# Kernel tuning notes

Hardware: AMD Instinct MI355X
Metric: run time of the kernel (lower is better)

Reference implementation:

```python
import jax, jax.numpy as jnp
import numpy as np


def setup_inputs() -> dict:
    key = jax.random.key(0)
    kq, kk, kv = jax.random.split(key, 3)
    B, S, D = 4, 4096, 64
    q = jax.random.normal(kq, (B, S, D), dtype=jnp.float32)
    k = jax.random.normal(kk, (B, S, D), dtype=jnp.float32)
    v = jax.random.normal(kv, (B, S, D), dtype=jnp.float32)
    return {"q": q, "k": k, "v": v}


def reference(q, k, v):
    # q,k,v: [B,S,D]. Faithful to the torch module:
    #   attn = softmax(q @ k^T / sqrt(D))  -- softmax over full row (NOT pre-masked)
    #   attn = attn.masked_fill(tril==0, 0.0)  -- post-softmax causal zeroing
    #   out  = attn @ v
    S = q.shape[1]
    d = jnp.sqrt(jnp.asarray(q.shape[-1], dtype=q.dtype))
    scores = jnp.einsum("bqd,bkd->bqk", q, k) / d  # [B,S,S]
    attn = jax.nn.softmax(scores, axis=-1)
    # causal tril mask sliced from the registered buffer mask[:S,:S]
    causal = jnp.tril(jnp.ones((S, S), dtype=bool))  # [S,S]
    attn = jnp.where(causal[None, :, :], attn, jnp.asarray(0.0, dtype=attn.dtype))
    out = jnp.einsum("bqk,bkd->bqd", attn, v)  # [B,S,D]
    return out
```

## Files before the change

kernel.cpp:

```cpp
#include <hip/hip_runtime.h>
#include <math.h>


typedef _Float16 f16;
typedef __attribute__((ext_vector_type(8))) _Float16 f16x8;
typedef __attribute__((ext_vector_type(16))) float f32x16;

constexpr int S = 4096, D = 64, TK = 32;
constexpr int B_ = 4;
constexpr int NKT = S / TK;
constexpr int QB = 32;
constexpr int WPB = 8;
constexpr int TPW = NKT / WPB;
constexpr int LDV = 40;
constexpr float QSC = 0.125f * 1.44269504088896340736f;

__global__ __launch_bounds__(256) void prep(
    const float* __restrict__ K, const float* __restrict__ V,
    f16* __restrict__ Kfrag, f16* __restrict__ Vfrag) {
  const int bx = blockIdx.x, tid = threadIdx.x;
  if (bx < B_ * NKT) {
    const float* src = K + (size_t)bx * TK * D;
    const int key = tid >> 3, j = tid & 7;
    float4 f0 = *reinterpret_cast<const float4*>(src + key * D + j * 8);
    float4 f1 = *reinterpret_cast<const float4*>(src + key * D + j * 8 + 4);
    f16x8 h;
    h[0] = (f16)f0.x; h[1] = (f16)f0.y; h[2] = (f16)f0.z; h[3] = (f16)f0.w;
    h[4] = (f16)f1.x; h[5] = (f16)f1.y; h[6] = (f16)f1.z; h[7] = (f16)f1.w;
    const int kc = j >> 1, h2 = j & 1;
    const int lane = key + 32 * h2;
    *reinterpret_cast<f16x8*>(Kfrag + ((size_t)bx * 4 + kc) * 512 + lane * 8) = h;
  } else {
    __shared__ float t32[TK][D + 4];
    const int vb = bx - B_ * NKT;
    const float* src = V + (size_t)vb * TK * D;
    #pragma unroll
    for (int r = 0; r < 2; ++r) {
      int f4 = tid + r * 256;
      int row = f4 >> 4, c4 = (f4 & 15) * 4;
      *reinterpret_cast<float4*>(&t32[row][c4]) =
          *reinterpret_cast<const float4*>(src + row * D + c4);
    }
    __syncthreads();
    const int dn = tid >> 7, kc2 = (tid >> 6) & 1, lane = tid & 63;
    const int l31 = lane & 31, h2 = lane >> 5;
    const int dim = dn * 32 + l31;
    const int k0 = kc2 * 16 + 8 * h2;
    f16x8 h;
    #pragma unroll
    for (int jj = 0; jj < 8; ++jj) h[jj] = (f16)t32[k0 + jj][dim];
    *reinterpret_cast<f16x8*>(
        Vfrag + ((size_t)vb * 4 + dn * 2 + kc2) * 512 + lane * 8) = h;
  }
}

__global__ __launch_bounds__(512, 4)
void attn(const float* __restrict__ Q, const f16* __restrict__ Kfrag,
          const f16* __restrict__ Vfrag, float* __restrict__ O) {
  __shared__ union {
    f16 ps[WPB][QB][LDV];
    struct { float nb[4][QB][68]; float db[WPB][QB]; } r;
  } sm;

  const int i = blockIdx.x;
  const int b = (i & 7) >> 1;
  const int t = ((i >> 3) << 1) | (i & 1);
  const int qb = (t & 1) ? (127 - (t >> 1)) : (t >> 1);
  const int q0 = qb * QB;

  const int tid = threadIdx.x;
  const int w = tid >> 6, lane = tid & 63;
  const int l31 = lane & 31, h2 = lane >> 5;

  const size_t bSD = (size_t)b * S * D;

  f16x8 qh[4], qlo[4];
  {
    const float* qr = Q + bSD + (size_t)(q0 + l31) * D;
    #pragma unroll
    for (int kc = 0; kc < 4; ++kc) {
      float4 f0 = *reinterpret_cast<const float4*>(qr + kc * 16 + 8 * h2);
      float4 f1 = *reinterpret_cast<const float4*>(qr + kc * 16 + 8 * h2 + 4);
      float f[8] = {f0.x, f0.y, f0.z, f0.w, f1.x, f1.y, f1.z, f1.w};
      #pragma unroll
      for (int j = 0; j < 8; ++j) {
        float v = f[j] * QSC;
        f16 hi = (f16)v;
        qh[kc][j] = hi;
        qlo[kc][j] = (f16)(v - (float)hi);
      }
    }
  }

  const f16* kf = Kfrag + (size_t)b * NKT * 2048 + lane * 8;
  const f16* vf = Vfrag + (size_t)b * NKT * 2048 + lane * 8;

  f32x16 on0, on1;
  float ls[16];
  #pragma unroll
  for (int r = 0; r < 16; ++r) { on0[r] = 0.f; on1[r] = 0.f; ls[r] = 0.f; }

  for (int j = 0; j < TPW; ++j) {
    const int kt = (j << 3) | w;
    const int kbase = kt * TK;
    const bool pv = (kbase <= q0);
    const bool diag = (kbase == q0);

    f16x8 v00, v01, v10, v11;
    if (pv) {
      const f16* vp = vf + (size_t)kt * 2048;
      v00 = *reinterpret_cast<const f16x8*>(vp);
      v01 = *reinterpret_cast<const f16x8*>(vp + 512);
      v10 = *reinterpret_cast<const f16x8*>(vp + 1024);
      v11 = *reinterpret_cast<const f16x8*>(vp + 1536);
    }

    const f16* kp = kf + (size_t)kt * 2048;
    f16x8 bk0 = *reinterpret_cast<const f16x8*>(kp);
    f16x8 bk1 = *reinterpret_cast<const f16x8*>(kp + 512);
    f16x8 bk2 = *reinterpret_cast<const f16x8*>(kp + 1024);
    f16x8 bk3 = *reinterpret_cast<const f16x8*>(kp + 1536);

    f32x16 acc;
    #pragma unroll
    for (int r = 0; r < 16; ++r) acc[r] = 0.f;
    acc = __builtin_amdgcn_mfma_f32_32x32x16_f16(qlo[0], bk0, acc, 0, 0, 0);
    acc = __builtin_amdgcn_mfma_f32_32x32x16_f16(qh[0],  bk0, acc, 0, 0, 0);
    acc = __builtin_amdgcn_mfma_f32_32x32x16_f16(qlo[1], bk1, acc, 0, 0, 0);
    acc = __builtin_amdgcn_mfma_f32_32x32x16_f16(qh[1],  bk1, acc, 0, 0, 0);
    acc = __builtin_amdgcn_mfma_f32_32x32x16_f16(qlo[2], bk2, acc, 0, 0, 0);
    acc = __builtin_amdgcn_mfma_f32_32x32x16_f16(qh[2],  bk2, acc, 0, 0, 0);
    acc = __builtin_amdgcn_mfma_f32_32x32x16_f16(qlo[3], bk3, acc, 0, 0, 0);
    acc = __builtin_amdgcn_mfma_f32_32x32x16_f16(qh[3],  bk3, acc, 0, 0, 0);

    #pragma unroll
    for (int r = 0; r < 16; ++r) {
      float pp = __builtin_amdgcn_exp2f(acc[r]);
      f16 ph = (f16)pp;
      ls[r] += (float)ph;
      if (pv) {
        const int row = (r & 3) + 8 * (r >> 2) + 4 * h2;
        sm.ps[w][row][l31] = (!diag || l31 <= row) ? ph : (f16)0.f;
      }
    }

    if (pv) {
      asm volatile("s_waitcnt lgkmcnt(0)" ::: "memory");
      f16x8 ap0 = *reinterpret_cast<const f16x8*>(&sm.ps[w][l31][8 * h2]);
      f16x8 ap1 = *reinterpret_cast<const f16x8*>(&sm.ps[w][l31][16 + 8 * h2]);
      on0 = __builtin_amdgcn_mfma_f32_32x32x16_f16(ap0, v00, on0, 0, 0, 0);
      on0 = __builtin_amdgcn_mfma_f32_32x32x16_f16(ap1, v01, on0, 0, 0, 0);
      on1 = __builtin_amdgcn_mfma_f32_32x32x16_f16(ap0, v10, on1, 0, 0, 0);
      on1 = __builtin_amdgcn_mfma_f32_32x32x16_f16(ap1, v11, on1, 0, 0, 0);
    }
  }

  #pragma unroll
  for (int r = 0; r < 16; ++r) {
    float v = ls[r];
    #pragma unroll
    for (int x = 1; x <= 16; x <<= 1) v += __shfl_xor(v, x);
    ls[r] = v;
  }
  __syncthreads();
  if (l31 == 0) {
    #pragma unroll
    for (int r = 0; r < 16; ++r)
      sm.r.db[w][(r & 3) + 8 * (r >> 2) + 4 * h2] = ls[r];
  }
  if (w < 4) {
    #pragma unroll
    for (int r = 0; r < 16; ++r) {
      const int row = (r & 3) + 8 * (r >> 2) + 4 * h2;
      sm.r.nb[w][row][l31]      = on0[r];
      sm.r.nb[w][row][32 + l31] = on1[r];
    }
  }
  __syncthreads();
  if (w >= 4) {
    #pragma unroll
    for (int r = 0; r < 16; ++r) {
      const int row = (r & 3) + 8 * (r >> 2) + 4 * h2;
      sm.r.nb[w - 4][row][l31]      += on0[r];
      sm.r.nb[w - 4][row][32 + l31] += on1[r];
    }
  }
  __syncthreads();

  const int row = tid >> 4, c4 = (tid & 15) * 4;
  float dsum = 0.f;
  #pragma unroll
  for (int ww = 0; ww < WPB; ++ww) dsum += sm.r.db[ww][row];
  const float inv = 1.f / dsum;
  float4 a0 = *reinterpret_cast<const float4*>(&sm.r.nb[0][row][c4]);
  float4 a1 = *reinterpret_cast<const float4*>(&sm.r.nb[1][row][c4]);
  float4 a2 = *reinterpret_cast<const float4*>(&sm.r.nb[2][row][c4]);
  float4 a3 = *reinterpret_cast<const float4*>(&sm.r.nb[3][row][c4]);
  float4 o;
  o.x = (a0.x + a1.x + a2.x + a3.x) * inv;
  o.y = (a0.y + a1.y + a2.y + a3.y) * inv;
  o.z = (a0.z + a1.z + a2.z + a3.z) * inv;
  o.w = (a0.w + a1.w + a2.w + a3.w) * inv;
  *reinterpret_cast<float4*>(O + bSD + (size_t)(q0 + row) * D + c4) = o;
}

extern "C" void kernel_launch(void* const* d_in, const int* in_sizes, int n_in,
                              void* d_out, int out_size, void* d_ws, size_t ws_size,
                              hipStream_t stream) {
  const float* q = (const float*)d_in[0];
  const float* k = (const float*)d_in[1];
  const float* v = (const float*)d_in[2];
  float* o = (float*)d_out;

  f16* Kfrag = (f16*)d_ws;
  f16* Vfrag = Kfrag + (size_t)B_ * S * D;

  prep<<<dim3(2 * B_ * NKT), dim3(256), 0, stream>>>(k, v, Kfrag, Vfrag);
  attn<<<dim3(512), dim3(512), 0, stream>>>(q, Kfrag, Vfrag, o);
}
```

Baseline: 111.3 us.

## Merge paired causal query tiles into one 1024-thread block

Each block now handles two 32-row query tiles, a low one and its mirrored high one (g and 127-g), with 16 waves. Waves alternate between the two tiles, and each half splits the key tiles across eight waves. The grid shrinks from 512 to 256 blocks, about one per CU, so the causal workload is balanced inside each block rather than across blocks. In exchange, the final reduction runs in two serialized passes with extra barriers, and the larger launch bound may tighten register limits.

```diff
diff --git a/kernel.cpp b/kernel.cpp
--- a/kernel.cpp
+++ b/kernel.cpp
@@ -9,9 +9,8 @@
 constexpr int S = 4096, D = 64, TK = 32;
 constexpr int B_ = 4;
 constexpr int NKT = S / TK;
-constexpr int QB = 32;
-constexpr int WPB = 8;
-constexpr int TPW = NKT / WPB;
+constexpr int WPB = 16;
+constexpr int TPW = 16;
 constexpr int LDV = 40;
 constexpr float QSC = 0.125f * 1.44269504088896340736f;
 
@@ -54,23 +53,25 @@
   }
 }
 
-__global__ __launch_bounds__(512, 4)
+__global__ __launch_bounds__(1024, 4)
 void attn(const float* __restrict__ Q, const f16* __restrict__ Kfrag,
           const f16* __restrict__ Vfrag, float* __restrict__ O) {
   __shared__ union {
-    f16 ps[WPB][QB][LDV];
-    struct { float nb[4][QB][68]; float db[WPB][QB]; } r;
+    f16 ps[WPB][32][LDV];
+    struct { float nb[4][32][68]; float db[2][8][32]; } r;
   } sm;
 
   const int i = blockIdx.x;
   const int b = (i & 7) >> 1;
   const int t = ((i >> 3) << 1) | (i & 1);
-  const int qb = (t & 1) ? (127 - (t >> 1)) : (t >> 1);
-  const int q0 = qb * QB;
 
   const int tid = threadIdx.x;
   const int w = tid >> 6, lane = tid & 63;
   const int l31 = lane & 31, h2 = lane >> 5;
+  const int qt = w & 1;
+  const int kidx = w >> 1;
+  const int g = qt ? (127 - t) : t;
+  const int q0 = g * TK;
 
   const size_t bSD = (size_t)b * S * D;
 
@@ -101,7 +102,7 @@
   for (int r = 0; r < 16; ++r) { on0[r] = 0.f; on1[r] = 0.f; ls[r] = 0.f; }
 
   for (int j = 0; j < TPW; ++j) {
-    const int kt = (j << 3) | w;
+    const int kt = (j << 3) | kidx;
     const int kbase = kt * TK;
     const bool pv = (kbase <= q0);
     const bool diag = (kbase == q0);
@@ -166,42 +167,50 @@
   if (l31 == 0) {
     #pragma unroll
     for (int r = 0; r < 16; ++r)
-      sm.r.db[w][(r & 3) + 8 * (r >> 2) + 4 * h2] = ls[r];
-  }
-  if (w < 4) {
-    #pragma unroll
-    for (int r = 0; r < 16; ++r) {
-      const int row = (r & 3) + 8 * (r >> 2) + 4 * h2;
-      sm.r.nb[w][row][l31]      = on0[r];
-      sm.r.nb[w][row][32 + l31] = on1[r];
-    }
-  }
-  __syncthreads();
-  if (w >= 4) {
-    #pragma unroll
-    for (int r = 0; r < 16; ++r) {
-      const int row = (r & 3) + 8 * (r >> 2) + 4 * h2;
-      sm.r.nb[w - 4][row][l31]      += on0[r];
-      sm.r.nb[w - 4][row][32 + l31] += on1[r];
-    }
-  }
-  __syncthreads();
-
-  const int row = tid >> 4, c4 = (tid & 15) * 4;
-  float dsum = 0.f;
+      sm.r.db[qt][w >> 1][(r & 3) + 8 * (r >> 2) + 4 * h2] = ls[r];
+  }
+
   #pragma unroll
-  for (int ww = 0; ww < WPB; ++ww) dsum += sm.r.db[ww][row];
-  const float inv = 1.f / dsum;
-  float4 a0 = *reinterpret_cast<const float4*>(&sm.r.nb[0][row][c4]);
-  float4 a1 = *reinterpret_cast<const float4*>(&sm.r.nb[1][row][c4]);
-  float4 a2 = *reinterpret_cast<const float4*>(&sm.r.nb[2][row][c4]);
-  float4 a3 = *reinterpret_cast<const float4*>(&sm.r.nb[3][row][c4]);
-  float4 o;
-  o.x = (a0.x + a1.x + a2.x + a3.x) * inv;
-  o.y = (a0.y + a1.y + a2.y + a3.y) * inv;
-  o.z = (a0.z + a1.z + a2.z + a3.z) * inv;
-  o.w = (a0.w + a1.w + a2.w + a3.w) * inv;
-  *reinterpret_cast<float4*>(O + bSD + (size_t)(q0 + row) * D + c4) = o;
+  for (int pass = 0; pass < 2; ++pass) {
+    const int slot = (w >> 1) & 3;
+    if (qt == pass && w < 8) {
+      #pragma unroll
+      for (int r = 0; r < 16; ++r) {
+        const int row = (r & 3) + 8 * (r >> 2) + 4 * h2;
+        sm.r.nb[slot][row][l31]      = on0[r];
+        sm.r.nb[slot][row][32 + l31] = on1[r];
+      }
+    }
+    __syncthreads();
+    if (qt == pass && w >= 8) {
+      #pragma unroll
+      for (int r = 0; r < 16; ++r) {
+        const int row = (r & 3) + 8 * (r >> 2) + 4 * h2;
+        sm.r.nb[slot][row][l31]      += on0[r];
+        sm.r.nb[slot][row][32 + l31] += on1[r];
+      }
+    }
+    __syncthreads();
+    if (tid < 512) {
+      const int row = tid >> 4, c4 = (tid & 15) * 4;
+      float dsum = 0.f;
+      #pragma unroll
+      for (int s = 0; s < 8; ++s) dsum += sm.r.db[pass][s][row];
+      const float inv = 1.f / dsum;
+      float4 a0 = *reinterpret_cast<const float4*>(&sm.r.nb[0][row][c4]);
+      float4 a1 = *reinterpret_cast<const float4*>(&sm.r.nb[1][row][c4]);
+      float4 a2 = *reinterpret_cast<const float4*>(&sm.r.nb[2][row][c4]);
+      float4 a3 = *reinterpret_cast<const float4*>(&sm.r.nb[3][row][c4]);
+      float4 o;
+      o.x = (a0.x + a1.x + a2.x + a3.x) * inv;
+      o.y = (a0.y + a1.y + a2.y + a3.y) * inv;
+      o.z = (a0.z + a1.z + a2.z + a3.z) * inv;
+      o.w = (a0.w + a1.w + a2.w + a3.w) * inv;
+      const int gp = pass ? (127 - t) : t;
+      *reinterpret_cast<float4*>(O + bSD + (size_t)(gp * TK + row) * D + c4) = o;
+    }
+    __syncthreads();
+  }
 }
 
 extern "C" void kernel_launch(void* const* d_in, const int* in_sizes, int n_in,
@@ -216,5 +225,5 @@
   f16* Vfrag = Kfrag + (size_t)B_ * S * D;
 
   prep<<<dim3(2 * B_ * NKT), dim3(256), 0, stream>>>(k, v, Kfrag, Vfrag);
-  attn<<<dim3(512), dim3(512), 0, stream>>>(q, Kfrag, Vfrag, o);
+  attn<<<dim3(256), dim3(1024), 0, stream>>>(q, Kfrag, Vfrag, o);
 }
```

New measurement: 109.7 us. No clear change (-1.4%).
